# Kernel optimization log

Hardware: AMD Instinct MI355X
Metric: run time of the kernel (lower is better)

## Reference

```python
import jax, jax.numpy as jnp
import numpy as np
import math

CHUNK = 128


def setup_inputs() -> dict:
    key = jax.random.key(0)
    ks = jax.random.split(key, 12)
    B, S, H, D = 2, 4096, 1024, 2048  # D = hidden_dim * expansion_factor
    std = 0.02
    inp = {
        "hidden_states": jax.random.normal(ks[0], (B, S, H), jnp.float32),
        "Wq": jax.random.normal(ks[1], (H, D), jnp.float32) * std,
        "bq": jnp.zeros((D,), jnp.float32),
        "Wk": jax.random.normal(ks[2], (H, D), jnp.float32) * std,
        "bk": jnp.zeros((D,), jnp.float32),
        "Wv": jax.random.normal(ks[3], (H, D), jnp.float32) * std,
        "bv": jnp.zeros((D,), jnp.float32),
        "Wg": jax.random.normal(ks[4], (H, D), jnp.float32) * std,
        "bg": jnp.zeros((D,), jnp.float32),
        "Wo": jax.random.normal(ks[5], (D, H), jnp.float32) * std,
        "bo": jnp.zeros((H,), jnp.float32),
    }
    return inp


def reference(hidden_states, Wq, bq, Wk, bk, Wv, bv, Wg, bg, Wo, bo):
    B, S, H = hidden_states.shape
    D = Wq.shape[1]
    cs = CHUNK
    nC = S // cs  # seq_len chosen as multiple of chunk_size (no padding path)

    q = hidden_states @ Wq + bq
    k = hidden_states @ Wk + bk
    v = hidden_states @ Wv + bv
    gate = jax.nn.sigmoid(hidden_states @ Wg + bg)

    qc = q.reshape(B, nC, cs, D)
    kc = k.reshape(B, nC, cs, D)
    vc = v.reshape(B, nC, cs, D)
    gc = gate.reshape(B, nC, cs, D)

    # intra-chunk causal softmax attention (vectorized over all chunks)
    scale = 1.0 / math.sqrt(D)
    attn = jnp.einsum('bncd,bnkd->bnck', qc, kc) * scale  # [B,nC,cs,cs]
    causal = jnp.tril(jnp.ones((cs, cs), bool))
    attn = jnp.where(causal, attn, -jnp.inf)
    attn = jax.nn.softmax(attn, axis=-1)
    local = jnp.einsum('bnck,bnkd->bncd', attn, vc)

    # inter-chunk linear-attention state accumulation:
    # cross_i = q_i @ sum_{j<i} K_j^T V_j  (sequential scan over chunks)
    def step(state, xs):
        qi, ki, vi = xs  # each [B,cs,D]
        cross = jnp.einsum('bcd,bde->bce', qi, state)
        state = state + jnp.einsum('bcd,bce->bde', ki, vi)
        return state, cross

    state0 = jnp.zeros((B, D, D), hidden_states.dtype)
    _, cross = jax.lax.scan(
        step, state0,
        (qc.transpose(1, 0, 2, 3), kc.transpose(1, 0, 2, 3), vc.transpose(1, 0, 2, 3)))
    cross = cross.transpose(1, 0, 2, 3)  # [B,nC,cs,D]

    out = (local + cross) * gc
    out = out.reshape(B, S, D)
    return out @ Wo + bo
```

## Files before the change

### kernel.cpp

```cpp
#include <hip/hip_runtime.h>
#include <hip/hip_bf16.h>
#include <math.h>


typedef __bf16 bf16_t;
typedef __bf16 bf16x8 __attribute__((ext_vector_type(8)));
typedef __bf16 bf16x4 __attribute__((ext_vector_type(4)));
typedef float f32x4 __attribute__((ext_vector_type(4)));

#define NB_ 2
#define SEQ 4096
#define HID 1024
#define DD 2048
#define BS 8192
#define LDS256 131072
#define LDS128 98304

__device__ __forceinline__ void async16(const void* g, void* l) {
  __builtin_amdgcn_global_load_lds(
      (const __attribute__((address_space(1))) void*)g,
      (__attribute__((address_space(3))) void*)l, 16, 0, 0);
}

#define VMW(n) asm volatile("s_waitcnt vmcnt(" #n ")" ::: "memory")
#define BARR __builtin_amdgcn_s_barrier()
#define FEN asm volatile("" ::: "memory")

template <int MFH>
__device__ __forceinline__ void readA8(const bf16_t* bufA, int aBase, int s0, int s1,
                                       bf16x8 (&af)[4][2]) {
#pragma unroll
  for (int mm = 0; mm < 4; ++mm) {
    int p = aBase + MFH * 8192 + mm * 1024;
    af[mm][0] = *reinterpret_cast<const bf16x8*>(&bufA[p + s0]);
    af[mm][1] = *reinterpret_cast<const bf16x8*>(&bufA[p + s1]);
  }
}
template <int NFH>
__device__ __forceinline__ void readB4(const bf16_t* bufB, int bBase, int s0, int s1,
                                       bf16x8 (&bv)[2][2]) {
#pragma unroll
  for (int nn = 0; nn < 2; ++nn) {
    int p = bBase + NFH * 8192 + nn * 1024;
    bv[nn][0] = *reinterpret_cast<const bf16x8*>(&bufB[p + s0]);
    bv[nn][1] = *reinterpret_cast<const bf16x8*>(&bufB[p + s1]);
  }
}
template <int MROWS, int MQ, int NQ>
__device__ __forceinline__ void mfmaQ(const bf16x8 (&af)[4][2], const bf16x8 (&bv)[2][2],
                                      f32x4 (&acc)[MROWS][4]) {
  __builtin_amdgcn_s_setprio(1);
#pragma unroll
  for (int kki = 0; kki < 2; ++kki)
#pragma unroll
    for (int mm = 0; mm < 4; ++mm)
#pragma unroll
      for (int nn = 0; nn < 2; ++nn)
        acc[MQ * 4 + mm][NQ * 2 + nn] = __builtin_amdgcn_mfma_f32_16x16x32_bf16(
            af[mm][kki], bv[nn][kki], acc[MQ * 4 + mm][NQ * 2 + nn], 0, 0, 0);
  __builtin_amdgcn_s_setprio(0);
}

__device__ __forceinline__ void core256(const bf16_t* __restrict__ A, int lda,
                                        const bf16_t* __restrict__ B, int ldb, int nt,
                                        bf16_t* lds, f32x4 (&acc)[8][4]) {
  const int t = threadIdx.x;
  const int lane = t & 63, w = t >> 6;
  const int wm = w >> 2, wn = w & 3;
  const int lr = lane & 15, lg = lane >> 4;
  const int xm = lr & 7;
  const int aBase = (wm * 64 + lr) * 64;
  const int bBase = (wn * 32 + lr) * 64;
  const int s0 = (lg ^ xm) * 8, s1 = ((4 + lg) ^ xm) * 8;
  const int slog = ((t & 7) ^ ((t >> 3) & 7)) * 8;
  int srcA[4], srcB[4];
#pragma unroll
  for (int blk = 0; blk < 4; ++blk) {
    int rA = ((blk & 1) << 7) + ((blk >> 1) << 6) + (t >> 3);
    int prB = (blk << 6) + (t >> 3);
    int rB = (((prB >> 5) & 3) << 6) + ((prB >> 7) << 5) + (prB & 31);
    srcA[blk] = rA * lda + slog;
    srcB[blk] = rB * ldb + slog;
  }
  const int dstT = t * 8;
#pragma unroll
  for (int m = 0; m < 8; ++m)
#pragma unroll
    for (int n = 0; n < 4; ++n) acc[m][n] = (f32x4){0.f, 0.f, 0.f, 0.f};

  {
    bf16_t* nA = lds;
    bf16_t* nB = lds + 16384;
    async16(A + srcA[0], nA + dstT);
    async16(A + srcA[1], nA + 4096 + dstT);
    async16(B + srcB[0], nB + dstT);
    async16(B + srcB[1], nB + 4096 + dstT);
    async16(A + srcA[2], nA + 8192 + dstT);
    async16(A + srcA[3], nA + 12288 + dstT);
    async16(B + srcB[2], nB + 8192 + dstT);
    async16(B + srcB[3], nB + 12288 + dstT);
  }
  bf16x8 af0[4][2], af1[4][2], bv0[2][2], bv1[2][2];
  for (int kt = 0; kt < nt; ++kt) {
    bf16_t* bufA = lds + ((kt & 1) << 15);
    bf16_t* bufB = bufA + 16384;
    bf16_t* nA = lds + (((kt + 1) & 1) << 15);
    bf16_t* nB = nA + 16384;
    const int kn = (kt + 1 < nt ? kt + 1 : 0) << 6;
    const bf16_t* An = A + kn;
    const bf16_t* Bn = B + kn;
    VMW(2); BARR; FEN;
    readA8<0>(bufA, aBase, s0, s1, af0);
    readB4<0>(bufB, bBase, s0, s1, bv0);
    readA8<1>(bufA, aBase, s0, s1, af1);
    async16(An + srcA[0], nA + dstT);
    async16(An + srcA[1], nA + 4096 + dstT);
    mfmaQ<8, 0, 0>(af0, bv0, acc);
    VMW(2); BARR; FEN;
    readB4<1>(bufB, bBase, s0, s1, bv1);
    async16(Bn + srcB[0], nB + dstT);
    async16(Bn + srcB[1], nB + 4096 + dstT);
    mfmaQ<8, 1, 0>(af1, bv0, acc);
    async16(An + srcA[2], nA + 8192 + dstT);
    async16(An + srcA[3], nA + 12288 + dstT);
    mfmaQ<8, 1, 1>(af1, bv1, acc);
    async16(Bn + srcB[2], nB + 8192 + dstT);
    async16(Bn + srcB[3], nB + 12288 + dstT);
    mfmaQ<8, 0, 1>(af0, bv1, acc);
  }
  VMW(0);
  BARR;
}

__device__ __forceinline__ void core128(const bf16_t* __restrict__ A, int lda,
                                        const bf16_t* __restrict__ B, int ldb, int nt,
                                        bf16_t* lds, f32x4 (&acc)[4][4]) {
  const int t = threadIdx.x;
  const int lane = t & 63, w = t >> 6;
  const int wm = w >> 2, wn = w & 3;
  const int lr = lane & 15, lg = lane >> 4;
  const int xm = lr & 7;
  const int aBase = (wm * 64 + lr) * 64;
  const int bBase = (wn * 32 + lr) * 64;
  const int s0 = (lg ^ xm) * 8, s1 = ((4 + lg) ^ xm) * 8;
  const int slog = ((t & 7) ^ ((t >> 3) & 7)) * 8;
  int srcA[2], srcB[4];
#pragma unroll
  for (int blk = 0; blk < 2; ++blk) srcA[blk] = (blk * 64 + (t >> 3)) * lda + slog;
#pragma unroll
  for (int blk = 0; blk < 4; ++blk) {
    int prB = (blk << 6) + (t >> 3);
    int rB = (((prB >> 5) & 3) << 6) + ((prB >> 7) << 5) + (prB & 31);
    srcB[blk] = rB * ldb + slog;
  }
  const int dstT = t * 8;
#pragma unroll
  for (int m = 0; m < 4; ++m)
#pragma unroll
    for (int n = 0; n < 4; ++n) acc[m][n] = (f32x4){0.f, 0.f, 0.f, 0.f};

  {
    bf16_t* nA = lds;
    bf16_t* nB = lds + 8192;
    async16(A + srcA[0], nA + dstT);
    async16(A + srcA[1], nA + 4096 + dstT);
    async16(B + srcB[0], nB + dstT);
    async16(B + srcB[1], nB + 4096 + dstT);
    async16(B + srcB[2], nB + 8192 + dstT);
    async16(B + srcB[3], nB + 12288 + dstT);
  }
  bf16x8 af[4][2], bv0[2][2], bv1[2][2];
  for (int kt = 0; kt < nt; ++kt) {
    bf16_t* bufA = lds + (kt & 1) * 24576;
    bf16_t* bufB = bufA + 8192;
    bf16_t* nA = lds + ((kt + 1) & 1) * 24576;
    bf16_t* nB = nA + 8192;
    const int kn = (kt + 1 < nt ? kt + 1 : 0) << 6;
    const bf16_t* An = A + kn;
    const bf16_t* Bn = B + kn;
    VMW(2); BARR; FEN;
    readA8<0>(bufA, aBase, s0, s1, af);
    readB4<0>(bufB, bBase, s0, s1, bv0);
    async16(An + srcA[0], nA + dstT);
    async16(An + srcA[1], nA + 4096 + dstT);
    async16(Bn + srcB[0], nB + dstT);
    mfmaQ<4, 0, 0>(af, bv0, acc);
    VMW(3); BARR; FEN;
    readB4<1>(bufB, bBase, s0, s1, bv1);
    async16(Bn + srcB[1], nB + 4096 + dstT);
    async16(Bn + srcB[2], nB + 8192 + dstT);
    async16(Bn + srcB[3], nB + 12288 + dstT);
    mfmaQ<4, 0, 1>(af, bv1, acc);
  }
  VMW(0);
  BARR;
}

__global__ void k_cvt(const float4* __restrict__ in, bf16x4* __restrict__ out, int n4) {
  int i = blockIdx.x * blockDim.x + threadIdx.x;
  if (i < n4) {
    float4 v = in[i];
    bf16x4 o;
    o[0] = (bf16_t)v.x; o[1] = (bf16_t)v.y; o[2] = (bf16_t)v.z; o[3] = (bf16_t)v.w;
    out[i] = o;
  }
}

__global__ void k_tconv(const float* __restrict__ in, bf16_t* __restrict__ out,
                        int R, int C) {
  __shared__ bf16_t tile[64][65];
  int bc = blockIdx.x, br = blockIdx.y;
  int t = threadIdx.x;
  int c = t & 63, r0 = t >> 6;
#pragma unroll
  for (int rr = 0; rr < 64; rr += 4) {
    int r = rr + r0;
    tile[r][c] = (bf16_t)in[(long)(br * 64 + r) * C + bc * 64 + c];
  }
  __syncthreads();
#pragma unroll
  for (int rr = 0; rr < 64; rr += 4) {
    int r = rr + r0;
    out[(long)(bc * 64 + r) * R + br * 64 + c] = tile[c][r];
  }
}

__global__ void k_tbf16(const bf16_t* __restrict__ in, bf16_t* __restrict__ out,
                        int R, int C) {
  __shared__ bf16_t tile[64][65];
  long zoff = (long)blockIdx.z * R * C;
  in += zoff;
  out += zoff;
  int bc = blockIdx.x, br = blockIdx.y;
  int t = threadIdx.x;
  int c = t & 63, r0 = t >> 6;
#pragma unroll
  for (int rr = 0; rr < 64; rr += 4) {
    int r = rr + r0;
    tile[r][c] = in[(long)(br * 64 + r) * C + bc * 64 + c];
  }
  __syncthreads();
#pragma unroll
  for (int rr = 0; rr < 64; rr += 4) {
    int r = rr + r0;
    out[(long)(bc * 64 + r) * R + br * 64 + c] = tile[c][r];
  }
}

__global__ __launch_bounds__(512, 2) void k_gemm_qkvg(
    const bf16_t* __restrict__ hsb, const bf16_t* __restrict__ Wt4,
    const float* __restrict__ bq, const float* __restrict__ bk,
    const float* __restrict__ bv, const float* __restrict__ bg,
    bf16_t* __restrict__ out) {
  extern __shared__ bf16_t lds[];
  int c = blockIdx.x;
  int c2 = (c & 7) * 128 + (c >> 3);
  int mb = c2 >> 5, nb = c2 & 31;
  f32x4 acc[8][4];
  core256(hsb + (long)mb * 256 * HID, HID, Wt4 + (long)nb * 256 * HID, HID,
          HID / 64, lds, acc);
  const int t = threadIdx.x, lane = t & 63, w = t >> 6;
  const int wm = w >> 2, wn = w & 3, lr = lane & 15, lg = lane >> 4;
  int z = nb >> 3;
  const float* bias = z == 0 ? bq : z == 1 ? bk : z == 2 ? bv : bg;
  int colbase = (nb & 7) * 256 + wn * 64;
  float b4[4];
#pragma unroll
  for (int nf = 0; nf < 4; ++nf) b4[nf] = bias[colbase + nf * 16 + lr];
  bf16_t* O = out + (long)z * BS * DD;
#pragma unroll
  for (int mf = 0; mf < 8; ++mf)
#pragma unroll
    for (int reg = 0; reg < 4; ++reg) {
      long row = mb * 256 + wm * 128 + mf * 16 + lg * 4 + reg;
#pragma unroll
      for (int nf = 0; nf < 4; ++nf) {
        float v = acc[mf][nf][reg] + b4[nf];
        if (z == 3) v = 1.f / (1.f + __expf(-v));
        O[row * DD + colbase + nf * 16 + lr] = (bf16_t)v;
      }
    }
}

__global__ __launch_bounds__(512, 2) void k_pair(const bf16_t* __restrict__ Q,
                                                 const bf16_t* __restrict__ Kb,
                                                 bf16_t* __restrict__ P) {
  extern __shared__ bf16_t lds[];
  int p = blockIdx.x, b = blockIdx.y;
  int c = 0, base = 0;
  while (base + (c >> 1) + 1 <= p) { base += (c >> 1) + 1; ++c; }
  int jt = p - base;
  f32x4 acc[4][4];
  core128(Q + ((long)b * SEQ + (long)c * 128) * DD, DD,
          Kb + ((long)b * SEQ + (long)jt * 256) * DD, DD, DD / 64, lds, acc);
  const int t = threadIdx.x, lane = t & 63, w = t >> 6;
  const int wm = w >> 2, wn = w & 3, lr = lane & 15, lg = lane >> 4;
  bf16_t* Pt = P + ((long)b * SEQ + (long)c * 128) * (long)SEQ + (long)jt * 256;
  const bool hasDiag = (jt == (c >> 1));
  const int side = c & 1;
  const float scale = 0.02209708691207961f;
  float* smf = (float*)lds;
#pragma unroll
  for (int mf = 0; mf < 4; ++mf)
#pragma unroll
    for (int reg = 0; reg < 4; ++reg) {
      int row = wm * 64 + mf * 16 + lg * 4 + reg;
#pragma unroll
      for (int nf = 0; nf < 4; ++nf) {
        int col = wn * 64 + nf * 16 + lr;
        float v = acc[mf][nf][reg];
        if (hasDiag && ((col >> 7) == side)) {
          int cc = col & 127;
          float sv = v * scale;
          smf[row * 128 + ((cc + row) & 127)] = (cc <= row) ? sv : -1e30f;
        } else {
          Pt[(long)row * SEQ + col] = (bf16_t)v;
        }
      }
    }
  if (hasDiag) {
    __syncthreads();
    if (t < 128) {
      int r = t;
      float mx = -1e30f;
      for (int cc = 0; cc <= r; ++cc) mx = fmaxf(mx, smf[r * 128 + ((cc + r) & 127)]);
      float s = 0.f;
      for (int cc = 0; cc <= r; ++cc) s += __expf(smf[r * 128 + ((cc + r) & 127)] - mx);
      float inv = 1.f / s;
      for (int cc = 0; cc < 128; ++cc) {
        float v = (cc <= r) ? __expf(smf[r * 128 + ((cc + r) & 127)] - mx) * inv : 0.f;
        Pt[(long)r * SEQ + side * 128 + cc] = (bf16_t)v;
      }
    }
  }
}

__global__ __launch_bounds__(512, 2) void k_gemm2(const bf16_t* __restrict__ P,
                                                  const bf16_t* __restrict__ Vt,
                                                  const bf16_t* __restrict__ G,
                                                  bf16_t* __restrict__ OutPre) {
  extern __shared__ bf16_t lds[];
  int bid = blockIdx.x;
  int mq = 31 - (bid >> 4);
  int r2 = bid & 15;
  int nb = r2 >> 1, b = r2 & 1;
  f32x4 acc[4][4];
  core128(P + ((long)b * SEQ + (long)mq * 128) * (long)SEQ, SEQ,
          Vt + (long)b * DD * SEQ + (long)nb * 256 * SEQ, SEQ, (mq + 1) * 2, lds, acc);
  const int t = threadIdx.x, lane = t & 63, w = t >> 6;
  const int wm = w >> 2, wn = w & 3, lr = lane & 15, lg = lane >> 4;
#pragma unroll
  for (int mf = 0; mf < 4; ++mf)
#pragma unroll
    for (int reg = 0; reg < 4; ++reg) {
      long row = (long)b * SEQ + (long)mq * 128 + wm * 64 + mf * 16 + lg * 4 + reg;
#pragma unroll
      for (int nf = 0; nf < 4; ++nf) {
        long idx = row * DD + nb * 256 + wn * 64 + nf * 16 + lr;
        float g = (float)G[idx];
        OutPre[idx] = (bf16_t)(acc[mf][nf][reg] * g);
      }
    }
}

__global__ __launch_bounds__(512, 2) void k_gemm3(const bf16_t* __restrict__ OutPre,
                                                  const bf16_t* __restrict__ Wot,
                                                  const float* __restrict__ bo,
                                                  float* __restrict__ out) {
  extern __shared__ bf16_t lds[];
  int mb = blockIdx.x >> 2, nb = blockIdx.x & 3;
  f32x4 acc[4][4];
  core128(OutPre + (long)mb * 128 * DD, DD, Wot + (long)nb * 256 * DD, DD,
          DD / 64, lds, acc);
  const int t = threadIdx.x, lane = t & 63, w = t >> 6;
  const int wm = w >> 2, wn = w & 3, lr = lane & 15, lg = lane >> 4;
  int colbase = nb * 256 + wn * 64;
  float b4[4];
#pragma unroll
  for (int nf = 0; nf < 4; ++nf) b4[nf] = bo[colbase + nf * 16 + lr];
#pragma unroll
  for (int mf = 0; mf < 4; ++mf)
#pragma unroll
    for (int reg = 0; reg < 4; ++reg) {
      long row = mb * 128 + wm * 64 + mf * 16 + lg * 4 + reg;
#pragma unroll
      for (int nf = 0; nf < 4; ++nf)
        out[row * HID + colbase + nf * 16 + lr] = acc[mf][nf][reg] + b4[nf];
    }
}

extern "C" void kernel_launch(void* const* d_in, const int* in_sizes, int n_in,
                              void* d_out, int out_size, void* d_ws, size_t ws_size,
                              hipStream_t stream) {
  const float* hs = (const float*)d_in[0];
  const float* Wq = (const float*)d_in[1];
  const float* bq = (const float*)d_in[2];
  const float* Wk = (const float*)d_in[3];
  const float* bk = (const float*)d_in[4];
  const float* Wv = (const float*)d_in[5];
  const float* bv = (const float*)d_in[6];
  const float* Wg = (const float*)d_in[7];
  const float* bg = (const float*)d_in[8];
  const float* Wo = (const float*)d_in[9];
  const float* bo = (const float*)d_in[10];
  float* out = (float*)d_out;

  char* ws = (char*)d_ws;
  const size_t MB = 1024 * 1024;
  bf16_t* P = (bf16_t*)(ws);
  bf16_t* hsb = (bf16_t*)(ws);
  bf16_t* Wt4 = (bf16_t*)(ws + 16 * MB);
  bf16_t* Wot = (bf16_t*)(ws + 64 * MB);
  bf16_t* QKVG = (bf16_t*)(ws + 68 * MB);
  bf16_t* Vt = (bf16_t*)(ws + 196 * MB);

  bf16_t* Qb = QKVG;
  bf16_t* Kbuf = QKVG + (long)BS * DD;
  bf16_t* Vbuf = QKVG + 2l * BS * DD;
  bf16_t* Gbuf = QKVG + 3l * BS * DD;
  bf16_t* OutPre = Vbuf;

  hipFuncSetAttribute((const void*)k_gemm_qkvg,
                      hipFuncAttributeMaxDynamicSharedMemorySize, LDS256);
  hipFuncSetAttribute((const void*)k_pair,
                      hipFuncAttributeMaxDynamicSharedMemorySize, LDS128);
  hipFuncSetAttribute((const void*)k_gemm2,
                      hipFuncAttributeMaxDynamicSharedMemorySize, LDS128);
  hipFuncSetAttribute((const void*)k_gemm3,
                      hipFuncAttributeMaxDynamicSharedMemorySize, LDS128);

  k_cvt<<<(BS * HID / 4 + 255) / 256, 256, 0, stream>>>((const float4*)hs,
                                                        (bf16x4*)hsb, BS * HID / 4);
  k_tconv<<<dim3(DD / 64, HID / 64), 256, 0, stream>>>(Wq, Wt4 + 0l * DD * HID, HID, DD);
  k_tconv<<<dim3(DD / 64, HID / 64), 256, 0, stream>>>(Wk, Wt4 + 1l * DD * HID, HID, DD);
  k_tconv<<<dim3(DD / 64, HID / 64), 256, 0, stream>>>(Wv, Wt4 + 2l * DD * HID, HID, DD);
  k_tconv<<<dim3(DD / 64, HID / 64), 256, 0, stream>>>(Wg, Wt4 + 3l * DD * HID, HID, DD);
  k_tconv<<<dim3(HID / 64, DD / 64), 256, 0, stream>>>(Wo, Wot, DD, HID);

  k_gemm_qkvg<<<1024, 512, LDS256, stream>>>(hsb, Wt4, bq, bk, bv, bg, QKVG);

  k_tbf16<<<dim3(DD / 64, SEQ / 64, NB_), 256, 0, stream>>>(Vbuf, Vt, SEQ, DD);

  k_pair<<<dim3(272, 2), 512, LDS128, stream>>>(Qb, Kbuf, P);

  k_gemm2<<<512, 512, LDS128, stream>>>(P, Vt, Gbuf, OutPre);

  k_gemm3<<<256, 512, LDS128, stream>>>(OutPre, Wot, bo, out);
}
```

Measured before the change: 433.1 us.

## Stage GEMM epilogues through LDS for coalesced stores and shrink QKVG tiles

```diff
diff --git a/kernel.cpp b/kernel.cpp
--- a/kernel.cpp
+++ b/kernel.cpp
@@ -13,8 +13,8 @@
 #define HID 1024
 #define DD 2048
 #define BS 8192
-#define LDS256 131072
-#define LDS128 98304
+#define LDS_CORE 98304
+#define SP 264
 
 __device__ __forceinline__ void async16(const void* g, void* l) {
   __builtin_amdgcn_global_load_lds(
@@ -59,77 +59,6 @@
         acc[MQ * 4 + mm][NQ * 2 + nn] = __builtin_amdgcn_mfma_f32_16x16x32_bf16(
             af[mm][kki], bv[nn][kki], acc[MQ * 4 + mm][NQ * 2 + nn], 0, 0, 0);
   __builtin_amdgcn_s_setprio(0);
-}
-
-__device__ __forceinline__ void core256(const bf16_t* __restrict__ A, int lda,
-                                        const bf16_t* __restrict__ B, int ldb, int nt,
-                                        bf16_t* lds, f32x4 (&acc)[8][4]) {
-  const int t = threadIdx.x;
-  const int lane = t & 63, w = t >> 6;
-  const int wm = w >> 2, wn = w & 3;
-  const int lr = lane & 15, lg = lane >> 4;
-  const int xm = lr & 7;
-  const int aBase = (wm * 64 + lr) * 64;
-  const int bBase = (wn * 32 + lr) * 64;
-  const int s0 = (lg ^ xm) * 8, s1 = ((4 + lg) ^ xm) * 8;
-  const int slog = ((t & 7) ^ ((t >> 3) & 7)) * 8;
-  int srcA[4], srcB[4];
-#pragma unroll
-  for (int blk = 0; blk < 4; ++blk) {
-    int rA = ((blk & 1) << 7) + ((blk >> 1) << 6) + (t >> 3);
-    int prB = (blk << 6) + (t >> 3);
-    int rB = (((prB >> 5) & 3) << 6) + ((prB >> 7) << 5) + (prB & 31);
-    srcA[blk] = rA * lda + slog;
-    srcB[blk] = rB * ldb + slog;
-  }
-  const int dstT = t * 8;
-#pragma unroll
-  for (int m = 0; m < 8; ++m)
-#pragma unroll
-    for (int n = 0; n < 4; ++n) acc[m][n] = (f32x4){0.f, 0.f, 0.f, 0.f};
-
-  {
-    bf16_t* nA = lds;
-    bf16_t* nB = lds + 16384;
-    async16(A + srcA[0], nA + dstT);
-    async16(A + srcA[1], nA + 4096 + dstT);
-    async16(B + srcB[0], nB + dstT);
-    async16(B + srcB[1], nB + 4096 + dstT);
-    async16(A + srcA[2], nA + 8192 + dstT);
-    async16(A + srcA[3], nA + 12288 + dstT);
-    async16(B + srcB[2], nB + 8192 + dstT);
-    async16(B + srcB[3], nB + 12288 + dstT);
-  }
-  bf16x8 af0[4][2], af1[4][2], bv0[2][2], bv1[2][2];
-  for (int kt = 0; kt < nt; ++kt) {
-    bf16_t* bufA = lds + ((kt & 1) << 15);
-    bf16_t* bufB = bufA + 16384;
-    bf16_t* nA = lds + (((kt + 1) & 1) << 15);
-    bf16_t* nB = nA + 16384;
-    const int kn = (kt + 1 < nt ? kt + 1 : 0) << 6;
-    const bf16_t* An = A + kn;
-    const bf16_t* Bn = B + kn;
-    VMW(2); BARR; FEN;
-    readA8<0>(bufA, aBase, s0, s1, af0);
-    readB4<0>(bufB, bBase, s0, s1, bv0);
-    readA8<1>(bufA, aBase, s0, s1, af1);
-    async16(An + srcA[0], nA + dstT);
-    async16(An + srcA[1], nA + 4096 + dstT);
-    mfmaQ<8, 0, 0>(af0, bv0, acc);
-    VMW(2); BARR; FEN;
-    readB4<1>(bufB, bBase, s0, s1, bv1);
-    async16(Bn + srcB[0], nB + dstT);
-    async16(Bn + srcB[1], nB + 4096 + dstT);
-    mfmaQ<8, 1, 0>(af1, bv0, acc);
-    async16(An + srcA[2], nA + 8192 + dstT);
-    async16(An + srcA[3], nA + 12288 + dstT);
-    mfmaQ<8, 1, 1>(af1, bv1, acc);
-    async16(Bn + srcB[2], nB + 8192 + dstT);
-    async16(Bn + srcB[3], nB + 12288 + dstT);
-    mfmaQ<8, 0, 1>(af0, bv1, acc);
-  }
-  VMW(0);
-  BARR;
 }
 
 __device__ __forceinline__ void core128(const bf16_t* __restrict__ A, int lda,
@@ -254,32 +183,42 @@
     bf16_t* __restrict__ out) {
   extern __shared__ bf16_t lds[];
   int c = blockIdx.x;
-  int c2 = (c & 7) * 128 + (c >> 3);
-  int mb = c2 >> 5, nb = c2 & 31;
-  f32x4 acc[8][4];
-  core256(hsb + (long)mb * 256 * HID, HID, Wt4 + (long)nb * 256 * HID, HID,
+  int r = c >> 9, xj = c & 511;
+  int xcd = xj & 7, j = xj >> 3;
+  int mb = r * 16 + (xcd & 1) * 8 + (j & 7);
+  int nb = (xcd >> 1) * 8 + (j >> 3);
+  f32x4 acc[4][4];
+  core128(hsb + (long)mb * 128 * HID, HID, Wt4 + (long)nb * 256 * HID, HID,
           HID / 64, lds, acc);
   const int t = threadIdx.x, lane = t & 63, w = t >> 6;
   const int wm = w >> 2, wn = w & 3, lr = lane & 15, lg = lane >> 4;
   int z = nb >> 3;
   const float* bias = z == 0 ? bq : z == 1 ? bk : z == 2 ? bv : bg;
-  int colbase = (nb & 7) * 256 + wn * 64;
+  int colT = (nb & 7) * 256;
   float b4[4];
 #pragma unroll
-  for (int nf = 0; nf < 4; ++nf) b4[nf] = bias[colbase + nf * 16 + lr];
-  bf16_t* O = out + (long)z * BS * DD;
-#pragma unroll
-  for (int mf = 0; mf < 8; ++mf)
+  for (int nf = 0; nf < 4; ++nf) b4[nf] = bias[colT + wn * 64 + nf * 16 + lr];
+#pragma unroll
+  for (int mf = 0; mf < 4; ++mf)
 #pragma unroll
     for (int reg = 0; reg < 4; ++reg) {
-      long row = mb * 256 + wm * 128 + mf * 16 + lg * 4 + reg;
+      int lrow = wm * 64 + mf * 16 + lg * 4 + reg;
 #pragma unroll
       for (int nf = 0; nf < 4; ++nf) {
         float v = acc[mf][nf][reg] + b4[nf];
         if (z == 3) v = 1.f / (1.f + __expf(-v));
-        O[row * DD + colbase + nf * 16 + lr] = (bf16_t)v;
+        lds[lrow * SP + wn * 64 + nf * 16 + lr] = (bf16_t)v;
       }
     }
+  __syncthreads();
+  bf16_t* O = out + (long)z * BS * DD + (long)mb * 128 * DD + colT;
+#pragma unroll
+  for (int it = 0; it < 8; ++it) {
+    int s = it * 512 + t;
+    int rr2 = s >> 5, sg = s & 31;
+    bf16x8 v = *reinterpret_cast<const bf16x8*>(&lds[rr2 * SP + sg * 8]);
+    *reinterpret_cast<bf16x8*>(&O[(long)rr2 * DD + sg * 8]) = v;
+  }
 }
 
 __global__ __launch_bounds__(512, 2) void k_pair(const bf16_t* __restrict__ Q,
@@ -299,26 +238,46 @@
   const bool hasDiag = (jt == (c >> 1));
   const int side = c & 1;
   const float scale = 0.02209708691207961f;
-  float* smf = (float*)lds;
 #pragma unroll
   for (int mf = 0; mf < 4; ++mf)
 #pragma unroll
     for (int reg = 0; reg < 4; ++reg) {
-      int row = wm * 64 + mf * 16 + lg * 4 + reg;
+      int lrow = wm * 64 + mf * 16 + lg * 4 + reg;
 #pragma unroll
       for (int nf = 0; nf < 4; ++nf) {
         int col = wn * 64 + nf * 16 + lr;
         float v = acc[mf][nf][reg];
-        if (hasDiag && ((col >> 7) == side)) {
-          int cc = col & 127;
-          float sv = v * scale;
-          smf[row * 128 + ((cc + row) & 127)] = (cc <= row) ? sv : -1e30f;
-        } else {
-          Pt[(long)row * SEQ + col] = (bf16_t)v;
+        if (hasDiag && (((col >> 7) == side) || side == 0)) v = 0.f;
+        lds[lrow * SP + col] = (bf16_t)v;
+      }
+    }
+  __syncthreads();
+#pragma unroll
+  for (int it = 0; it < 8; ++it) {
+    int s = it * 512 + t;
+    int rr2 = s >> 5, sg = s & 31;
+    bf16x8 v = *reinterpret_cast<const bf16x8*>(&lds[rr2 * SP + sg * 8]);
+    *reinterpret_cast<bf16x8*>(&Pt[(long)rr2 * SEQ + sg * 8]) = v;
+  }
+  if (hasDiag) {
+    VMW(0);
+    __syncthreads();
+    float* smf = (float*)lds;
+#pragma unroll
+    for (int mf = 0; mf < 4; ++mf)
+#pragma unroll
+      for (int reg = 0; reg < 4; ++reg) {
+        int row = wm * 64 + mf * 16 + lg * 4 + reg;
+#pragma unroll
+        for (int nf = 0; nf < 4; ++nf) {
+          int col = wn * 64 + nf * 16 + lr;
+          if ((col >> 7) == side) {
+            int cc = col & 127;
+            float sv = acc[mf][nf][reg] * scale;
+            smf[row * 128 + ((cc + row) & 127)] = (cc <= row) ? sv : -1e30f;
+          }
         }
       }
-    }
-  if (hasDiag) {
     __syncthreads();
     if (t < 128) {
       int r = t;
@@ -349,18 +308,28 @@
           Vt + (long)b * DD * SEQ + (long)nb * 256 * SEQ, SEQ, (mq + 1) * 2, lds, acc);
   const int t = threadIdx.x, lane = t & 63, w = t >> 6;
   const int wm = w >> 2, wn = w & 3, lr = lane & 15, lg = lane >> 4;
+  long rowb = (long)b * SEQ + (long)mq * 128;
 #pragma unroll
   for (int mf = 0; mf < 4; ++mf)
 #pragma unroll
     for (int reg = 0; reg < 4; ++reg) {
-      long row = (long)b * SEQ + (long)mq * 128 + wm * 64 + mf * 16 + lg * 4 + reg;
+      int lrow = wm * 64 + mf * 16 + lg * 4 + reg;
 #pragma unroll
       for (int nf = 0; nf < 4; ++nf) {
-        long idx = row * DD + nb * 256 + wn * 64 + nf * 16 + lr;
-        float g = (float)G[idx];
-        OutPre[idx] = (bf16_t)(acc[mf][nf][reg] * g);
+        int col = wn * 64 + nf * 16 + lr;
+        float g = (float)G[(rowb + lrow) * DD + nb * 256 + col];
+        lds[lrow * SP + col] = (bf16_t)(acc[mf][nf][reg] * g);
       }
     }
+  __syncthreads();
+  bf16_t* O = OutPre + rowb * DD + nb * 256;
+#pragma unroll
+  for (int it = 0; it < 8; ++it) {
+    int s = it * 512 + t;
+    int rr2 = s >> 5, sg = s & 31;
+    bf16x8 v = *reinterpret_cast<const bf16x8*>(&lds[rr2 * SP + sg * 8]);
+    *reinterpret_cast<bf16x8*>(&O[(long)rr2 * DD + sg * 8]) = v;
+  }
 }
 
 __global__ __launch_bounds__(512, 2) void k_gemm3(const bf16_t* __restrict__ OutPre,
@@ -421,13 +390,13 @@
   bf16_t* OutPre = Vbuf;
 
   hipFuncSetAttribute((const void*)k_gemm_qkvg,
-                      hipFuncAttributeMaxDynamicSharedMemorySize, LDS256);
+                      hipFuncAttributeMaxDynamicSharedMemorySize, LDS_CORE);
   hipFuncSetAttribute((const void*)k_pair,
-                      hipFuncAttributeMaxDynamicSharedMemorySize, LDS128);
+                      hipFuncAttributeMaxDynamicSharedMemorySize, LDS_CORE);
   hipFuncSetAttribute((const void*)k_gemm2,
-                      hipFuncAttributeMaxDynamicSharedMemorySize, LDS128);
+                      hipFuncAttributeMaxDynamicSharedMemorySize, LDS_CORE);
   hipFuncSetAttribute((const void*)k_gemm3,
-                      hipFuncAttributeMaxDynamicSharedMemorySize, LDS128);
+                      hipFuncAttributeMaxDynamicSharedMemorySize, LDS_CORE);
 
   k_cvt<<<(BS * HID / 4 + 255) / 256, 256, 0, stream>>>((const float4*)hs,
                                                         (bf16x4*)hsb, BS * HID / 4);
@@ -437,13 +406,13 @@
   k_tconv<<<dim3(DD / 64, HID / 64), 256, 0, stream>>>(Wg, Wt4 + 3l * DD * HID, HID, DD);
   k_tconv<<<dim3(HID / 64, DD / 64), 256, 0, stream>>>(Wo, Wot, DD, HID);
 
-  k_gemm_qkvg<<<1024, 512, LDS256, stream>>>(hsb, Wt4, bq, bk, bv, bg, QKVG);
+  k_gemm_qkvg<<<2048, 512, LDS_CORE, stream>>>(hsb, Wt4, bq, bk, bv, bg, QKVG);
 
   k_tbf16<<<dim3(DD / 64, SEQ / 64, NB_), 256, 0, stream>>>(Vbuf, Vt, SEQ, DD);
 
-  k_pair<<<dim3(272, 2), 512, LDS128, stream>>>(Qb, Kbuf, P);
-
-  k_gemm2<<<512, 512, LDS128, stream>>>(P, Vt, Gbuf, OutPre);
-
-  k_gemm3<<<256, 512, LDS128, stream>>>(OutPre, Wot, bo, out);
-}
+  k_pair<<<dim3(272, 2), 512, LDS_CORE, stream>>>(Qb, Kbuf, P);
+
+  k_gemm2<<<512, 512, LDS_CORE, stream>>>(P, Vt, Gbuf, OutPre);
+
+  k_gemm3<<<256, 512, LDS_CORE, stream>>>(OutPre, Wot, bo, out);
+}
```

Measured after the change: 446.6 us. 3.1% more time.
